# Kernel optimization log

Hardware: AMD Instinct MI355X
Metric: run time of the kernel (lower is better)

Reference implementation:

```python
import jax, jax.numpy as jnp
import numpy as np

DIM = 512; H = 8; HD = DIM // H
LAM = 4.0; NS_ITERS = 5; EPS = 1e-5
B = 2; S = 512


def setup_inputs() -> dict:
    key = jax.random.key(0)
    ks = jax.random.split(key, 3)
    return {
        "x": jax.random.normal(ks[0], (B, S, DIM), jnp.float32),
        "qkv_w": jax.random.normal(ks[1], (3 * DIM, DIM), jnp.float32) * 0.02,
        "qkv_b": jnp.zeros((3 * DIM,), jnp.float32),
        "proj_w": jax.random.normal(ks[2], (DIM, DIM), jnp.float32) * 0.02,
        "proj_b": jnp.zeros((DIM,), jnp.float32),
    }


def _ns_inverse(A, iters=NS_ITERS):
    # Newton-Schulz iterative matrix inverse: X <- X(2I - AX),
    # init X0 = A^T / (||A||_1 * ||A||_inf)
    n = A.shape[-1]
    I = jnp.eye(n, dtype=A.dtype)
    n1 = jnp.max(jnp.sum(jnp.abs(A), axis=-2), axis=-1)    # max column sum
    ninf = jnp.max(jnp.sum(jnp.abs(A), axis=-1), axis=-1)  # max row sum
    X = jnp.swapaxes(A, -2, -1) / (n1 * ninf)[..., None, None]
    for _ in range(iters):
        X = X @ (2.0 * I - A @ X)
    return X


def reference(x, qkv_w, qkv_b, proj_w, proj_b):
    Bb, Ss, C = x.shape
    qkv = x @ qkv_w.T + qkv_b                               # [B,S,3*DIM]
    qkv = qkv.reshape(Bb, Ss, 3, H, HD).transpose(2, 0, 3, 1, 4)
    q, k, v = qkv[0], qkv[1], qkv[2]                        # [B,H,S,HD]
    # Laplacian (L1) kernel: exp(-|q_i - k_j|_1 / lambda)
    l1 = jnp.sum(jnp.abs(q[:, :, :, None, :] - k[:, :, None, :, :]), axis=-1)
    W = jnp.exp(-l1 / LAM)                                  # [B,H,S,S]
    mask = jnp.tril(jnp.ones((Ss, Ss), dtype=x.dtype))      # causal mask
    W = W * mask
    W_inv = _ns_inverse(W)
    # whitening over (batch, query) dims; torch.var is unbiased (ddof=1)
    mu = jnp.mean(W, axis=(0, 2), keepdims=True)            # [1,H,1,S]
    var = jnp.var(W, axis=(0, 2), keepdims=True, ddof=1)
    W_norm = (W - mu) / jnp.sqrt(var + EPS)
    context = jnp.swapaxes(W, -2, -1) @ v                   # [B,H,S,HD]
    context = W_inv @ context
    ga = W_norm @ context                                   # [B,H,S,HD]
    ga = ga.transpose(0, 2, 1, 3).reshape(Bb, Ss, C)
    return ga @ proj_w.T + proj_b
```

## Files before the change

### kernel.cpp

```cpp
#include <hip/hip_runtime.h>

#define Bq 2
#define Hh 8
#define Ss 512
#define HD 64
#define DIM 512

using f32x4   = __attribute__((ext_vector_type(4))) float;
using bf16x8s = __attribute__((ext_vector_type(8))) short;
typedef _Float16 f16x8 __attribute__((ext_vector_type(8)));

__constant__ int d_tIs[36] = {0,1,1,2,2,2,3,3,3,3,4,4,4,4,4,5,5,5,5,5,5,6,6,6,6,6,6,6,7,7,7,7,7,7,7,7};
__constant__ int d_tJs[36] = {0,0,1,0,1,2,0,1,2,3,0,1,2,3,4,0,1,2,3,4,5,0,1,2,3,4,5,6,0,1,2,3,4,5,6,7};

__device__ __forceinline__ float bf2f(unsigned short u) {
    return __uint_as_float(((unsigned int)u) << 16);
}
__device__ __forceinline__ unsigned short f2bf(float f) {
    unsigned int u = __float_as_uint(f);
    u = (u + 0x7FFFu + ((u >> 16) & 1u)) >> 16;
    return (unsigned short)u;
}

__global__ __launch_bounds__(256) void mm64_k(
    const float* __restrict__ A, const float* __restrict__ B,
    const float* __restrict__ bias, float* __restrict__ C,
    int K, int ldc)
{
    const int row0 = blockIdx.y * 64, col0 = blockIdx.x * 64;
    __shared__ unsigned short AsH[64][40], AsL[64][40];
    __shared__ unsigned short BsH[64][40], BsL[64][40];
    const int t = threadIdx.x;
    const int wave = t >> 6, lane = t & 63;
    const int ln = lane & 15, quad = lane >> 4;

    f32x4 acc[4];
#pragma unroll
    for (int i = 0; i < 4; ++i) acc[i] = (f32x4){0.f, 0.f, 0.f, 0.f};

    const int sr = t >> 2, sg = (t & 3) * 8;

    for (int k0 = 0; k0 < K; k0 += 32) {
        __syncthreads();
#pragma unroll
        for (int half = 0; half < 2; ++half) {
            const float* src = half ? B : A;
            int base = half ? col0 : row0;
            const float* p = &src[(long)(base + sr) * K + k0 + sg];
            float4 f0 = *(const float4*)p;
            float4 f1 = *(const float4*)(p + 4);
            float fv[8] = {f0.x, f0.y, f0.z, f0.w, f1.x, f1.y, f1.z, f1.w};
            unsigned short hv[8], lv[8];
#pragma unroll
            for (int e = 0; e < 8; ++e) {
                hv[e] = f2bf(fv[e]);
                lv[e] = f2bf(fv[e] - bf2f(hv[e]));
            }
            uint4 H, L;
            H.x = hv[0] | (hv[1] << 16); H.y = hv[2] | (hv[3] << 16);
            H.z = hv[4] | (hv[5] << 16); H.w = hv[6] | (hv[7] << 16);
            L.x = lv[0] | (lv[1] << 16); L.y = lv[2] | (lv[3] << 16);
            L.z = lv[4] | (lv[5] << 16); L.w = lv[6] | (lv[7] << 16);
            if (!half) { *(uint4*)&AsH[sr][sg] = H; *(uint4*)&AsL[sr][sg] = L; }
            else       { *(uint4*)&BsH[sr][sg] = H; *(uint4*)&BsL[sr][sg] = L; }
        }
        __syncthreads();

        bf16x8s afH, afL, bfH[4], bfL[4];
        afH = *(const bf16x8s*)&AsH[wave * 16 + ln][quad * 8];
        afL = *(const bf16x8s*)&AsL[wave * 16 + ln][quad * 8];
#pragma unroll
        for (int nt = 0; nt < 4; ++nt) {
            bfH[nt] = *(const bf16x8s*)&BsH[nt * 16 + ln][quad * 8];
            bfL[nt] = *(const bf16x8s*)&BsL[nt * 16 + ln][quad * 8];
        }
#pragma unroll
        for (int nt = 0; nt < 4; ++nt) {
            acc[nt] = __builtin_amdgcn_mfma_f32_16x16x32_bf16(afH, bfH[nt], acc[nt], 0, 0, 0);
            acc[nt] = __builtin_amdgcn_mfma_f32_16x16x32_bf16(afH, bfL[nt], acc[nt], 0, 0, 0);
            acc[nt] = __builtin_amdgcn_mfma_f32_16x16x32_bf16(afL, bfH[nt], acc[nt], 0, 0, 0);
        }
    }

    const int gr0 = row0 + wave * 16 + quad * 4;
#pragma unroll
    for (int nt = 0; nt < 4; ++nt) {
        const int gc = col0 + nt * 16 + ln;
        float bb = bias[gc];
#pragma unroll
        for (int r = 0; r < 4; ++r)
            C[(long)(gr0 + r) * ldc + gc] = acc[nt][r] + bb;
    }
}

__global__ __launch_bounds__(256) void wt_fused(const float* __restrict__ qkv,
                                                _Float16* __restrict__ Wh,
                                                _Float16* __restrict__ Wt,
                                                _Float16* __restrict__ vT,
                                                float* __restrict__ rsum,
                                                float* __restrict__ rsq,
                                                float* __restrict__ csum)
{
    __shared__ float qs[32][64];
    __shared__ float ks[32][64];
    __shared__ float colacc[64];
    const int L = blockIdx.x;
    const int q = L & 7, s = L >> 3;
    const int z = 2 * q + (s >= 66 ? 1 : 0);
    const int bx = (s >= 66) ? s - 66 : s;
    int b = z >> 3, h = z & 7;
    int t = threadIdx.x;
    long zo = (long)z * Ss * Ss;

    if (bx >= 64) {
        float (*sT)[33] = (float(*)[33])qs;
        int dt = (bx - 64) * 32;
        int d = t & 31, kr = t >> 5;
        for (int kt = 0; kt < Ss; kt += 32) {
            __syncthreads();
#pragma unroll
            for (int p = 0; p < 4; ++p) {
                int kk = kr + p * 8;
                sT[kk][d] = qkv[(long)b * (Ss * 3 * DIM) + (long)(kt + kk) * (3 * DIM) + 2 * DIM + h * HD + dt + d];
            }
            __syncthreads();
#pragma unroll
            for (int p = 0; p < 4; ++p) {
                int dd = kr + p * 8;
                vT[(long)z * (HD * Ss) + (long)(dt + dd) * Ss + kt + d] = (_Float16)sT[d][dd];
            }
        }
        return;
    }

    int ti = bx >> 3, tj = bx & 7;
    int i0 = ti * 64, j0 = tj * 64;

    if (tj > ti) {
        if (t < 64) {
            rsum[((z * 8 + ti) * 512) + j0 + t] = 0.f;
            rsq [((z * 8 + ti) * 512) + j0 + t] = 0.f;
            csum[((z * 8 + tj) * 512) + i0 + t] = 0.f;
        }
        return;
    }

    int ia = (t & 15) * 4;
    int ja = (t >> 4) * 4;
    const float* qb = qkv + (long)b * Ss * (3 * DIM) + h * HD;
    const float* kb = qb + DIM;
    float acc[4][4] = {};

    for (int d0 = 0; d0 < 64; d0 += 32) {
        __syncthreads();
        int row = t & 63, dg = (t >> 6) * 8;
        float4 qv  = *(const float4*)&qb[(long)(i0 + row) * (3 * DIM) + d0 + dg];
        float4 qv2 = *(const float4*)&qb[(long)(i0 + row) * (3 * DIM) + d0 + dg + 4];
        float4 kv  = *(const float4*)&kb[(long)(j0 + row) * (3 * DIM) + d0 + dg];
        float4 kv2 = *(const float4*)&kb[(long)(j0 + row) * (3 * DIM) + d0 + dg + 4];
        qs[dg+0][row] = qv.x;  qs[dg+1][row] = qv.y;  qs[dg+2][row] = qv.z;  qs[dg+3][row] = qv.w;
        qs[dg+4][row] = qv2.x; qs[dg+5][row] = qv2.y; qs[dg+6][row] = qv2.z; qs[dg+7][row] = qv2.w;
        ks[dg+0][row] = kv.x;  ks[dg+1][row] = kv.y;  ks[dg+2][row] = kv.z;  ks[dg+3][row] = kv.w;
        ks[dg+4][row] = kv2.x; ks[dg+5][row] = kv2.y; ks[dg+6][row] = kv2.z; ks[dg+7][row] = kv2.w;
        __syncthreads();
#pragma unroll
        for (int d = 0; d < 32; ++d) {
            float4 q0 = *(const float4*)&qs[d][ia];
            float4 k0 = *(const float4*)&ks[d][ja];
            float qv_[4] = {q0.x, q0.y, q0.z, q0.w};
            float kv_[4] = {k0.x, k0.y, k0.z, k0.w};
#pragma unroll
            for (int aa = 0; aa < 4; ++aa)
#pragma unroll
                for (int c = 0; c < 4; ++c)
                    acc[aa][c] += fabsf(qv_[aa] - kv_[c]);
        }
    }

#pragma unroll
    for (int aa = 0; aa < 4; ++aa) {
        int i = i0 + ia + aa;
#pragma unroll
        for (int c = 0; c < 4; ++c) {
            int j = j0 + ja + c;
            float e = expf(-acc[aa][c] * 0.25f);
            acc[aa][c] = (j <= i) ? e : 0.0f;
        }
    }
#pragma unroll
    for (int c = 0; c < 4; ++c) {
        int j = j0 + ja + c;
        float rs = 0.f, rq = 0.f;
#pragma unroll
        for (int aa = 0; aa < 4; ++aa) { rs += acc[aa][c]; rq += acc[aa][c] * acc[aa][c]; }
        _Float16 ha[4] __attribute__((aligned(8))) = {(_Float16)acc[0][c], (_Float16)acc[1][c], (_Float16)acc[2][c], (_Float16)acc[3][c]};
        *(uint2*)&Wt[zo + (long)j * Ss + i0 + ia] = *(const uint2*)ha;
#pragma unroll
        for (int off = 8; off > 0; off >>= 1) {
            rs += __shfl_down(rs, off, 16);
            rq += __shfl_down(rq, off, 16);
        }
        if ((t & 15) == 0) {
            rsum[((z * 8 + ti) * 512) + j] = rs;
            rsq [((z * 8 + ti) * 512) + j] = rq;
        }
    }
#pragma unroll
    for (int aa = 0; aa < 4; ++aa) {
        int i = i0 + ia + aa;
        _Float16 hb[4] __attribute__((aligned(8))) = {(_Float16)acc[aa][0], (_Float16)acc[aa][1], (_Float16)acc[aa][2], (_Float16)acc[aa][3]};
        *(uint2*)&Wh[zo + (long)i * Ss + j0 + ja] = *(const uint2*)hb;
    }
    __syncthreads();
    if (t < 64) colacc[t] = 0.f;
    __syncthreads();
#pragma unroll
    for (int aa = 0; aa < 4; ++aa) {
        float cs = acc[aa][0] + acc[aa][1] + acc[aa][2] + acc[aa][3];
        atomicAdd(&colacc[ia + aa], cs);
    }
    __syncthreads();
    if (t < 64) csum[((z * 8 + tj) * 512) + i0 + t] = colacc[t];
}

__device__ __forceinline__ void wk_core(char* smc, const _Float16* A, const _Float16* B,
                                        long zA, long zB, int col0, int kbeg, int kend,
                                        f32x4* acc)
{
    _Float16 (*As0)[72] = (_Float16(*)[72])smc;
    _Float16 (*Bs0)[72] = (_Float16(*)[72])(smc + 9216);
    _Float16 (*As1)[72] = (_Float16(*)[72])(smc + 18432);
    _Float16 (*Bs1)[72] = (_Float16(*)[72])(smc + 27648);
    const int t = threadIdx.x;
    const int wave = t >> 6, lane = t & 63;
    const int ln = lane & 15, quad = lane >> 4;
    const int r2 = t >> 2, c2 = (t & 3) * 16;
    const long aoff = zA + (long)r2 * Ss;
    const long boff = zB + (long)(col0 + r2) * Ss;

    uint4 ua0 = *(const uint4*)&A[aoff + kbeg + c2];
    uint4 ua1 = *(const uint4*)&A[aoff + kbeg + c2 + 8];
    uint4 ub0 = *(const uint4*)&B[boff + kbeg + c2];
    uint4 ub1 = *(const uint4*)&B[boff + kbeg + c2 + 8];
    *(uint4*)&As0[r2][c2]     = ua0;
    *(uint4*)&As0[r2][c2 + 8] = ua1;
    *(uint4*)&Bs0[r2][c2]     = ub0;
    *(uint4*)&Bs0[r2][c2 + 8] = ub1;
    int cur = 0;
    for (int k0 = kbeg; k0 < kend; k0 += 64) {
        int kn = k0 + 64;
        if (kn < kend) {
            ua0 = *(const uint4*)&A[aoff + kn + c2];
            ua1 = *(const uint4*)&A[aoff + kn + c2 + 8];
            ub0 = *(const uint4*)&B[boff + kn + c2];
            ub1 = *(const uint4*)&B[boff + kn + c2 + 8];
        }
        __syncthreads();
        _Float16 (*As)[72] = cur ? As1 : As0;
        _Float16 (*Bs)[72] = cur ? Bs1 : Bs0;
#pragma unroll
        for (int kk = 0; kk < 64; kk += 32) {
            f16x8 af = *(const f16x8*)&As[wave * 16 + ln][quad * 8 + kk];
#pragma unroll
            for (int nt = 0; nt < 4; ++nt) {
                f16x8 bf = *(const f16x8*)&Bs[nt * 16 + ln][quad * 8 + kk];
                acc[nt] = __builtin_amdgcn_mfma_f32_16x16x32_f16(af, bf, acc[nt], 0, 0, 0);
            }
        }
        if (kn < kend) {
            _Float16 (*An)[72] = cur ? As0 : As1;
            _Float16 (*Bn)[72] = cur ? Bs0 : Bs1;
            *(uint4*)&An[r2][c2]     = ua0;
            *(uint4*)&An[r2][c2 + 8] = ua1;
            *(uint4*)&Bn[r2][c2]     = ub0;
            *(uint4*)&Bn[r2][c2 + 8] = ub1;
        }
        cur ^= 1;
    }
}

template<int HASA1>
__device__ __forceinline__ void wk_core32(char* smc, const float* A0, const float* A1,
                                          const _Float16* B, long zA, long zB, int col0,
                                          int kbeg, int kend, f32x4* acc)
{
    _Float16 (*As0)[40] = (_Float16(*)[40])smc;
    _Float16 (*Bs0)[40] = (_Float16(*)[40])(smc + 5120);
    _Float16 (*As1)[40] = (_Float16(*)[40])(smc + 10240);
    _Float16 (*Bs1)[40] = (_Float16(*)[40])(smc + 15360);
    const int t = threadIdx.x;
    const int wave = t >> 6, lane = t & 63;
    const int ln = lane & 15, quad = lane >> 4;
    const int r4 = t >> 2, c4 = (t & 3) * 8;
    const long aoff = zA + (long)r4 * Ss;
    const long boff = zB + (long)(col0 + r4) * Ss;

    float4 p0 = *(const float4*)&A0[aoff + kbeg + c4];
    float4 p1 = *(const float4*)&A0[aoff + kbeg + c4 + 4];
    float4 q0, q1;
    if constexpr (HASA1) {
        q0 = *(const float4*)&A1[aoff + kbeg + c4];
        q1 = *(const float4*)&A1[aoff + kbeg + c4 + 4];
    }
    uint4 ub = *(const uint4*)&B[boff + kbeg + c4];
    {
        _Float16 hv[8] __attribute__((aligned(16)));
        if constexpr (HASA1) {
            hv[0] = (_Float16)(p0.x + q0.x); hv[1] = (_Float16)(p0.y + q0.y);
            hv[2] = (_Float16)(p0.z + q0.z); hv[3] = (_Float16)(p0.w + q0.w);
            hv[4] = (_Float16)(p1.x + q1.x); hv[5] = (_Float16)(p1.y + q1.y);
            hv[6] = (_Float16)(p1.z + q1.z); hv[7] = (_Float16)(p1.w + q1.w);
        } else {
            hv[0] = (_Float16)p0.x; hv[1] = (_Float16)p0.y;
            hv[2] = (_Float16)p0.z; hv[3] = (_Float16)p0.w;
            hv[4] = (_Float16)p1.x; hv[5] = (_Float16)p1.y;
            hv[6] = (_Float16)p1.z; hv[7] = (_Float16)p1.w;
        }
        *(uint4*)&As0[r4][c4] = *(const uint4*)hv;
        *(uint4*)&Bs0[r4][c4] = ub;
    }
    int cur = 0;
    for (int k0 = kbeg; k0 < kend; k0 += 32) {
        int kn = k0 + 32;
        if (kn < kend) {
            p0 = *(const float4*)&A0[aoff + kn + c4];
            p1 = *(const float4*)&A0[aoff + kn + c4 + 4];
            if constexpr (HASA1) {
                q0 = *(const float4*)&A1[aoff + kn + c4];
                q1 = *(const float4*)&A1[aoff + kn + c4 + 4];
            }
            ub = *(const uint4*)&B[boff + kn + c4];
        }
        __syncthreads();
        _Float16 (*As)[40] = cur ? As1 : As0;
        _Float16 (*Bs)[40] = cur ? Bs1 : Bs0;
        f16x8 af = *(const f16x8*)&As[wave * 16 + ln][quad * 8];
#pragma unroll
        for (int nt = 0; nt < 4; ++nt) {
            f16x8 bf = *(const f16x8*)&Bs[nt * 16 + ln][quad * 8];
            acc[nt] = __builtin_amdgcn_mfma_f32_16x16x32_f16(af, bf, acc[nt], 0, 0, 0);
        }
        if (kn < kend) {
            _Float16 hv[8] __attribute__((aligned(16)));
            if constexpr (HASA1) {
                hv[0] = (_Float16)(p0.x + q0.x); hv[1] = (_Float16)(p0.y + q0.y);
                hv[2] = (_Float16)(p0.z + q0.z); hv[3] = (_Float16)(p0.w + q0.w);
                hv[4] = (_Float16)(p1.x + q1.x); hv[5] = (_Float16)(p1.y + q1.y);
                hv[6] = (_Float16)(p1.z + q1.z); hv[7] = (_Float16)(p1.w + q1.w);
            } else {
                hv[0] = (_Float16)p0.x; hv[1] = (_Float16)p0.y;
                hv[2] = (_Float16)p0.z; hv[3] = (_Float16)p0.w;
                hv[4] = (_Float16)p1.x; hv[5] = (_Float16)p1.y;
                hv[6] = (_Float16)p1.z; hv[7] = (_Float16)p1.w;
            }
            _Float16 (*An)[40] = cur ? As0 : As1;
            _Float16 (*Bn)[40] = cur ? Bs0 : Bs1;
            *(uint4*)&An[r4][c4] = *(const uint4*)hv;
            *(uint4*)&Bn[r4][c4] = ub;
        }
        cur ^= 1;
    }
}

__device__ __forceinline__ void sym_core(char* smc, const _Float16* A, long zo,
                                         int row0, int col0, int kend, f32x4* acc)
{
    _Float16 (*As0)[72] = (_Float16(*)[72])smc;
    _Float16 (*Bs0)[72] = (_Float16(*)[72])(smc + 9216);
    _Float16 (*As1)[72] = (_Float16(*)[72])(smc + 18432);
    _Float16 (*Bs1)[72] = (_Float16(*)[72])(smc + 27648);
    const int t = threadIdx.x;
    const int wave = t >> 6, lane = t & 63;
    const int ln = lane & 15, quad = lane >> 4;
    const int r2 = t >> 2, c2 = (t & 3) * 16;
    const long aoff = zo + (long)(row0 + r2) * Ss;
    const long boff = zo + (long)(col0 + r2) * Ss;
    uint4 ua0 = *(const uint4*)&A[aoff + c2];
    uint4 ua1 = *(const uint4*)&A[aoff + c2 + 8];
    uint4 ub0 = *(const uint4*)&A[boff + c2];
    uint4 ub1 = *(const uint4*)&A[boff + c2 + 8];
    *(uint4*)&As0[r2][c2]     = ua0;
    *(uint4*)&As0[r2][c2 + 8] = ua1;
    *(uint4*)&Bs0[r2][c2]     = ub0;
    *(uint4*)&Bs0[r2][c2 + 8] = ub1;
    int cur = 0;
    for (int k0 = 0; k0 < kend; k0 += 64) {
        int kn = k0 + 64;
        if (kn < kend) {
            ua0 = *(const uint4*)&A[aoff + kn + c2];
            ua1 = *(const uint4*)&A[aoff + kn + c2 + 8];
            ub0 = *(const uint4*)&A[boff + kn + c2];
            ub1 = *(const uint4*)&A[boff + kn + c2 + 8];
        }
        __syncthreads();
        _Float16 (*As)[72] = cur ? As1 : As0;
        _Float16 (*Bs)[72] = cur ? Bs1 : Bs0;
#pragma unroll
        for (int kk = 0; kk < 64; kk += 32) {
            f16x8 af = *(const f16x8*)&As[wave * 16 + ln][quad * 8 + kk];
#pragma unroll
            for (int nt = 0; nt < 4; ++nt) {
                f16x8 bf = *(const f16x8*)&Bs[nt * 16 + ln][quad * 8 + kk];
                acc[nt] = __builtin_amdgcn_mfma_f32_16x16x32_f16(af, bf, acc[nt], 0, 0, 0);
            }
        }
        if (kn < kend) {
            _Float16 (*An)[72] = cur ? As0 : As1;
            _Float16 (*Bn)[72] = cur ? Bs0 : Bs1;
            *(uint4*)&An[r2][c2]     = ua0;
            *(uint4*)&An[r2][c2 + 8] = ua1;
            *(uint4*)&Bn[r2][c2]     = ub0;
            *(uint4*)&Bn[r2][c2 + 8] = ub1;
        }
        cur ^= 1;
    }
}

__device__ __forceinline__ void sym_store_offdiag(char* smc, _Float16* T, long zo,
                                                  int row0, int col0,
                                                  const _Float16 (*ov)[4])
{
    _Float16 (*ltR)[72] = (_Float16(*)[72])smc;
    _Float16 (*ltT)[72] = (_Float16(*)[72])(smc + 9216);
    const int t = threadIdx.x;
    const int wave = t >> 6, lane = t & 63;
    const int ln = lane & 15, quad = lane >> 4;
    const int lr0 = wave * 16 + quad * 4;
    __syncthreads();
#pragma unroll
    for (int nt = 0; nt < 4; ++nt) {
        const int lc = nt * 16 + ln;
        *(uint2*)&ltT[lc][lr0] = *(const uint2*)ov[nt];
#pragma unroll
        for (int r = 0; r < 4; ++r)
            ltR[lr0 + r][lc] = ov[nt][r];
    }
    __syncthreads();
    const int tr = t >> 2, tcg = (t & 3) * 16;
    uint4 a0 = *(const uint4*)&ltR[tr][tcg];
    uint4 a1 = *(const uint4*)&ltR[tr][tcg + 8];
    _Float16* d0 = &T[zo + (long)(row0 + tr) * Ss + col0 + tcg];
    *(uint4*)&d0[0] = a0;
    *(uint4*)&d0[8] = a1;
    uint4 b0 = *(const uint4*)&ltT[tr][tcg];
    uint4 b1 = *(const uint4*)&ltT[tr][tcg + 8];
    _Float16* d1 = &T[zo + (long)(col0 + tr) * Ss + row0 + tcg];
    *(uint4*)&d1[0] = b0;
    *(uint4*)&d1[8] = b1;
}

__global__ __launch_bounds__(256) void mid_k(const _Float16* __restrict__ vT,
                                             const _Float16* __restrict__ Wt,
                                             float* __restrict__ y0,
                                             const float* __restrict__ rsum,
                                             const float* __restrict__ rsq,
                                             const float* __restrict__ csum,
                                             float* __restrict__ scal,
                                             float* __restrict__ mu,
                                             float* __restrict__ inv_sig,
                                             const _Float16* __restrict__ Wh,
                                             _Float16* __restrict__ U)
{
    __shared__ __align__(16) char sm[36864];
    int bx = blockIdx.x, t = threadIdx.x;
    if (bx < 128) {
        int q = bx & 7, s = bx >> 3;
        int z = 2 * q + (s >= 8 ? 1 : 0);
        int cc = s & 7;
        int col0 = cc * 64;
        long zA = (long)z * (HD * Ss), zB = (long)z * Ss * Ss;
        f32x4 acc[4];
#pragma unroll
        for (int i = 0; i < 4; ++i) acc[i] = (f32x4){0.f, 0.f, 0.f, 0.f};
        wk_core(sm, vT, Wt, zA, zB, col0, col0, Ss, acc);
        const int wave = t >> 6, lane = t & 63;
        const int ln = lane & 15, quad = lane >> 4;
        const int gr = wave * 16 + quad * 4;
#pragma unroll
        for (int nt = 0; nt < 4; ++nt) {
            const int gc = col0 + nt * 16 + ln;
#pragma unroll
            for (int r = 0; r < 4; ++r)
                y0[zA + (long)(gr + r) * Ss + gc] = acc[nt][r];
        }
    } else if (bx < 144) {
        int z = bx - 128;
        float* s1 = (float*)sm;
        float* s2 = s1 + 256;
        float mx1 = 0.f, mx2 = 0.f;
        for (int jj = t; jj < 512; jj += 256) {
            float rs = 0.f, cs = 0.f;
#pragma unroll
            for (int ti = 0; ti < 8; ++ti) {
                rs += rsum[(z * 8 + ti) * 512 + jj];
                cs += csum[(z * 8 + ti) * 512 + jj];
            }
            mx1 = fmaxf(mx1, rs);
            mx2 = fmaxf(mx2, cs);
        }
        s1[t] = mx1; s2[t] = mx2;
        __syncthreads();
        for (int off = 128; off > 0; off >>= 1) {
            if (t < off) {
                s1[t] = fmaxf(s1[t], s1[t + off]);
                s2[t] = fmaxf(s2[t], s2[t + off]);
            }
            __syncthreads();
        }
        if (t == 0) scal[z] = 1.0f / (s1[0] * s2[0]);
    } else if (bx < 152) {
        int h = bx - 144;
        for (int jj = t; jj < 512; jj += 256) {
            float s = 0.f, q = 0.f;
#pragma unroll
            for (int b = 0; b < 2; ++b)
#pragma unroll
                for (int ti = 0; ti < 8; ++ti) {
                    int zz = b * 8 + h;
                    s += rsum[(zz * 8 + ti) * 512 + jj];
                    q += rsq [(zz * 8 + ti) * 512 + jj];
                }
            float m_ = s / 1024.f;
            float var = (q - s * s / 1024.f) / 1023.f;
            inv_sig[h * 512 + jj] = 1.0f / sqrtf(var + 1e-5f);
            mu[h * 512 + jj] = m_;
        }
    } else {
        int u = bx - 152;
        int q = u & 7, s = u >> 3;
        int z = 2 * q + (s >= 36 ? 1 : 0);
        int tile = (s >= 36) ? s - 36 : s;
        const long zo = (long)z * Ss * Ss;
        const int ti = d_tIs[tile], tj = d_tJs[tile];
        const int row0 = ti * 64, col0 = tj * 64;
        f32x4 acc[4];
#pragma unroll
        for (int i = 0; i < 4; ++i) acc[i] = (f32x4){0.f, 0.f, 0.f, 0.f};
        sym_core(sm, Wh, zo, row0, col0, col0 + 64, acc);
        const int wave = t >> 6, lane = t & 63;
        const int ln = lane & 15, quad = lane >> 4;
        _Float16 ov[4][4] __attribute__((aligned(8)));
#pragma unroll
        for (int nt = 0; nt < 4; ++nt)
#pragma unroll
            for (int r = 0; r < 4; ++r)
                ov[nt][r] = (_Float16)acc[nt][r];
        if (ti == tj) {
            const int gr0 = row0 + wave * 16 + quad * 4;
#pragma unroll
            for (int nt = 0; nt < 4; ++nt) {
                const int gc = col0 + nt * 16 + ln;
#pragma unroll
                for (int r = 0; r < 4; ++r)
                    U[zo + (long)(gr0 + r) * Ss + gc] = ov[nt][r];
            }
        } else {
            sym_store_offdiag(sm, U, zo, row0, col0, ov);
        }
    }
}

template<int FIRST>
__global__ __launch_bounds__(256) void sq_k(const _Float16* __restrict__ Tc,
                                            _Float16* __restrict__ Tn,
                                            const float* __restrict__ Y0,
                                            const float* __restrict__ Y1,
                                            float* __restrict__ O0,
                                            float* __restrict__ O1,
                                            const float* __restrict__ scal)
{
    __shared__ __align__(16) char sm[36864];
    const int L = blockIdx.x;
    const int q = L & 7, s = L >> 3;
    const int z = 2 * q + (s >= 52 ? 1 : 0);
    const int x = (s >= 52) ? s - 52 : s;
    const int t = threadIdx.x;
    const int wave = t >> 6, lane = t & 63;
    const int ln = lane & 15, quad = lane >> 4;

    if (x < 36) {
        const long zo = (long)z * Ss * Ss;
        const int ti = d_tIs[x], tj = d_tJs[x];
        const int row0 = ti * 64, col0 = tj * 64;
        f32x4 acc[4];
#pragma unroll
        for (int i = 0; i < 4; ++i) acc[i] = (f32x4){0.f, 0.f, 0.f, 0.f};
        sym_core(sm, Tc, zo, row0, col0, Ss, acc);
        const float sv = FIRST ? scal[z] : 0.f;
        const int gr0 = row0 + wave * 16 + quad * 4;
        _Float16 ov[4][4] __attribute__((aligned(8)));
#pragma unroll
        for (int nt = 0; nt < 4; ++nt) {
            const int gc = col0 + nt * 16 + ln;
#pragma unroll
            for (int r = 0; r < 4; ++r) {
                const long gi = zo + (long)(gr0 + r) * Ss + gc;
                float val;
                if (FIRST) val = sv * sv * acc[nt][r] - 2.0f * sv * (float)Tc[gi];
                else       val = 2.0f * (float)Tc[gi] + acc[nt][r];
                ov[nt][r] = (_Float16)val;
            }
        }
        if (ti == tj) {
#pragma unroll
            for (int nt = 0; nt < 4; ++nt) {
                const int gc = col0 + nt * 16 + ln;
#pragma unroll
                for (int r = 0; r < 4; ++r)
                    Tn[zo + (long)(gr0 + r) * Ss + gc] = ov[nt][r];
            }
        } else {
            sym_store_offdiag(sm, Tn, zo, row0, col0, ov);
        }
    } else {
        const int bx = x - 36;
        const int cc = bx & 7, kh = bx >> 3;
        const int col0 = cc * 64;
        const long zA = (long)z * (HD * Ss);
        const long zB = (long)z * Ss * Ss;
        f32x4 acc[4];
#pragma unroll
        for (int i = 0; i < 4; ++i) acc[i] = (f32x4){0.f, 0.f, 0.f, 0.f};
        wk_core32<FIRST ? 0 : 1>(sm, Y0, Y1, Tc, zA, zB, col0, kh * 256, kh * 256 + 256, acc);
        const float alpha = FIRST ? -scal[z] : 1.0f;
        float* O = kh ? O1 : O0;
        const int gr = wave * 16 + quad * 4;
#pragma unroll
        for (int nt = 0; nt < 4; ++nt) {
            const int gc = col0 + nt * 16 + ln;
#pragma unroll
            for (int r = 0; r < 4; ++r) {
                const long idx = zA + (long)(gr + r) * Ss + gc;
                float val = alpha * acc[nt][r];
                if (kh == 0) {
                    if (FIRST) val += 2.0f * Y0[idx];
                    else       val += 2.0f * (Y0[idx] + Y1[idx]);
                }
                O[idx] = val;
            }
        }
    }
}

__global__ __launch_bounds__(256) void yk_k(const float* __restrict__ A0,
                                            const float* __restrict__ A1,
                                            const _Float16* __restrict__ T,
                                            float* __restrict__ O0,
                                            float* __restrict__ O1)
{
    __shared__ __align__(16) char sm[20480];
    const int L = blockIdx.x;
    const int q = L & 7, s = L >> 3;
    const int z = 2 * q + (s >= 16 ? 1 : 0);
    const int w = (s >= 16) ? s - 16 : s;
    const int cc = w & 7, kh = w >> 3;
    const int col0 = cc * 64;
    const long zA = (long)z * (HD * Ss);
    const long zB = (long)z * Ss * Ss;
    const int t = threadIdx.x;
    const int wave = t >> 6, lane = t & 63;
    const int ln = lane & 15, quad = lane >> 4;

    f32x4 acc[4];
#pragma unroll
    for (int i = 0; i < 4; ++i) acc[i] = (f32x4){0.f, 0.f, 0.f, 0.f};
    wk_core32<1>(sm, A0, A1, T, zA, zB, col0, kh * 256, kh * 256 + 256, acc);

    float* O = kh ? O1 : O0;
    const int gr = wave * 16 + quad * 4;
#pragma unroll
    for (int nt = 0; nt < 4; ++nt) {
        const int gc = col0 + nt * 16 + ln;
#pragma unroll
        for (int r = 0; r < 4; ++r) {
            const long idx = zA + (long)(gr + r) * Ss + gc;
            float val = acc[nt][r];
            if (kh == 0) val += 2.0f * (A0[idx] + A1[idx]);
            O[idx] = val;
        }
    }
}

__global__ __launch_bounds__(256) void c2s_k(const float* __restrict__ A0,
                                             const float* __restrict__ A1,
                                             const _Float16* __restrict__ Wt,
                                             _Float16* __restrict__ c2sT,
                                             const float* __restrict__ scal,
                                             const float* __restrict__ inv_sig,
                                             const float* __restrict__ mu,
                                             float* __restrict__ negopart)
{
    __shared__ __align__(16) char sm[20480];
    __shared__ float red[64];
    const int L = blockIdx.x;
    const int q = L & 7, sIdx = L >> 3;
    const int z = 2 * q + (sIdx >= 8 ? 1 : 0);
    const int cb = (sIdx >= 8) ? sIdx - 8 : sIdx;
    const int h = z & 7;
    const int col0 = cb * 64;
    const long zA = (long)z * (HD * Ss);
    const long zB = (long)z * Ss * Ss;
    const int t = threadIdx.x;
    const int wave = t >> 6, lane = t & 63;
    const int ln = lane & 15, quad = lane >> 4;

    f32x4 acc[4];
#pragma unroll
    for (int i = 0; i < 4; ++i) acc[i] = (f32x4){0.f, 0.f, 0.f, 0.f};
    wk_core32<1>(sm, A0, A1, Wt, zA, zB, col0, col0, Ss, acc);

    if (t < 64) red[t] = 0.f;
    __syncthreads();
    const int gr = wave * 16 + quad * 4;
    float pr[4] = {0.f, 0.f, 0.f, 0.f};
    float s = scal[z];
#pragma unroll
    for (int nt = 0; nt < 4; ++nt) {
        const int gc = col0 + nt * 16 + ln;
#pragma unroll
        for (int r = 0; r < 4; ++r) {
            float val = inv_sig[h * 512 + gc] * (s * acc[nt][r]);
            pr[r] += mu[h * 512 + gc] * val;
            c2sT[zA + (long)(gr + r) * Ss + gc] = (_Float16)val;
        }
    }
#pragma unroll
    for (int r = 0; r < 4; ++r)
        atomicAdd(&red[gr + r], pr[r]);
    __syncthreads();
    if (t < 64)
        negopart[(z * 8 + cb) * 64 + t] = red[t];
}

__global__ __launch_bounds__(256) void ga_k(const _Float16* __restrict__ Wh,
                                            const _Float16* __restrict__ c2sT,
                                            const float* __restrict__ negopart,
                                            float* __restrict__ gat)
{
    __shared__ __align__(16) char sm[36864];
    __shared__ float neg[64];
    const int L = blockIdx.x;
    const int q = L & 7, sIdx = L >> 3;
    const int z = 2 * q + (sIdx >= 8 ? 1 : 0);
    const int mb = (sIdx >= 8) ? sIdx - 8 : sIdx;
    const int b = z >> 3, h = z & 7;
    const int m0 = mb * 64;
    const long zA = (long)z * Ss * Ss;
    const long zB = (long)z * (HD * Ss);
    const int t = threadIdx.x;
    const int wave = t >> 6, lane = t & 63;
    const int ln = lane & 15, quad = lane >> 4;

    if (t < 64) {
        float s = 0.f;
#pragma unroll
        for (int k = 0; k < 8; ++k) s += negopart[(z * 8 + k) * 64 + t];
        neg[t] = s;
    }
    __syncthreads();

    f32x4 acc[4];
#pragma unroll
    for (int i = 0; i < 4; ++i) acc[i] = (f32x4){0.f, 0.f, 0.f, 0.f};
    wk_core(sm, c2sT, Wh, zB, zA, m0, 0, m0 + 64, acc);

    const int gr = wave * 16 + quad * 4;
#pragma unroll
    for (int nt = 0; nt < 4; ++nt) {
        const int m = m0 + nt * 16 + ln;
#pragma unroll
        for (int r = 0; r < 4; ++r) {
            const int d = gr + r;
            gat[(long)b * (Ss * DIM) + (long)m * DIM + h * HD + d] = acc[nt][r] - neg[d];
        }
    }
}

extern "C" void kernel_launch(void* const* d_in, const int* in_sizes, int n_in,
                              void* d_out, int out_size, void* d_ws, size_t ws_size,
                              hipStream_t stream)
{
    const float* x      = (const float*)d_in[0];
    const float* qkv_w  = (const float*)d_in[1];
    const float* qkv_b  = (const float*)d_in[2];
    const float* proj_w = (const float*)d_in[3];
    const float* proj_b = (const float*)d_in[4];
    float* out = (float*)d_out;
    float* ws  = (float*)d_ws;

    float* qkv     = ws;
    _Float16* Wh   = (_Float16*)(ws + 1572864);
    _Float16* Wt   = (_Float16*)(ws + 3670016);
    _Float16* vT   = (_Float16*)(ws + 5767168);
    _Float16* T[5];
    for (int i = 0; i < 5; ++i) T[i] = (_Float16*)(ws + 6029312 + (long)i * 2097152);
    float* Ya0 = ws + 16515072;
    float* Ya1 = ws + 17039360;
    float* Yb0 = ws + 17563648;
    float* Yb1 = ws + 18087936;
    _Float16* c2sT = (_Float16*)(ws + 19136512);
    float* rsum    = ws + 19398656;
    float* rsq     = ws + 19464192;
    float* csum    = ws + 19529728;
    float* scal    = ws + 19595264;
    float* mu      = ws + 19595280;
    float* inv_sig = ws + 19599376;
    float* negp    = ws + 19603472;
    float* gat     = ws + 19611664;

    dim3 blk(256);

    mm64_k<<<dim3(24, 16), blk, 0, stream>>>(x, qkv_w, qkv_b, qkv, DIM, 3 * DIM);

    wt_fused<<<dim3(1056), blk, 0, stream>>>(qkv, Wh, Wt, vT, rsum, rsq, csum);

    mid_k<<<dim3(728), blk, 0, stream>>>(vT, Wt, Ya0, rsum, rsq, csum, scal, mu, inv_sig,
                                         Wh, T[0]);

    sq_k<1><<<dim3(832), blk, 0, stream>>>(T[0], T[1], Ya0, nullptr, Yb0, Yb1, scal);
    sq_k<0><<<dim3(832), blk, 0, stream>>>(T[1], T[2], Yb0, Yb1,     Ya0, Ya1, scal);
    sq_k<0><<<dim3(832), blk, 0, stream>>>(T[2], T[3], Ya0, Ya1,     Yb0, Yb1, scal);
    sq_k<0><<<dim3(832), blk, 0, stream>>>(T[3], T[4], Yb0, Yb1,     Ya0, Ya1, scal);

    yk_k<<<dim3(256), blk, 0, stream>>>(Ya0, Ya1, T[4], Yb0, Yb1);

    c2s_k<<<dim3(128), blk, 0, stream>>>(Yb0, Yb1, Wt, c2sT, scal, inv_sig, mu, negp);

    ga_k<<<dim3(128), blk, 0, stream>>>(Wh, c2sT, negp, gat);

    mm64_k<<<dim3(8, 16), blk, 0, stream>>>(gat, proj_w, proj_b, out, DIM, DIM);
}
```

Baseline: 198.6 us.

## Launch only lower-triangular W tiles and widen wk_core32 K-step to 64

The W-building kernel now launches only the 36 causal (lower-triangular plus diagonal) 64x64 tiles per head, using lookup tables, instead of 64 tiles with early exit. Upper tiles no longer exist as blocks, so each lower-triangle block also zeroes the transposed partial-sum slots. The shared wk_core32 GEMM loop now stages 64-wide K chunks with a 72-element padded shared layout, halving the number of barrier and load phases. The price is more shared memory per block (36 KB) and more registers for prefetch buffers, which may reduce occupancy.

```diff
diff --git a/kernel.cpp b/kernel.cpp
--- a/kernel.cpp
+++ b/kernel.cpp
@@ -106,15 +106,15 @@
     __shared__ float colacc[64];
     const int L = blockIdx.x;
     const int q = L & 7, s = L >> 3;
-    const int z = 2 * q + (s >= 66 ? 1 : 0);
-    const int bx = (s >= 66) ? s - 66 : s;
+    const int z = 2 * q + (s >= 38 ? 1 : 0);
+    const int bx = (s >= 38) ? s - 38 : s;
     int b = z >> 3, h = z & 7;
     int t = threadIdx.x;
     long zo = (long)z * Ss * Ss;
 
-    if (bx >= 64) {
+    if (bx >= 36) {
         float (*sT)[33] = (float(*)[33])qs;
-        int dt = (bx - 64) * 32;
+        int dt = (bx - 36) * 32;
         int d = t & 31, kr = t >> 5;
         for (int kt = 0; kt < Ss; kt += 32) {
             __syncthreads();
@@ -133,16 +133,13 @@
         return;
     }
 
-    int ti = bx >> 3, tj = bx & 7;
-    int i0 = ti * 64, j0 = tj * 64;
-
-    if (tj > ti) {
-        if (t < 64) {
-            rsum[((z * 8 + ti) * 512) + j0 + t] = 0.f;
-            rsq [((z * 8 + ti) * 512) + j0 + t] = 0.f;
-            csum[((z * 8 + tj) * 512) + i0 + t] = 0.f;
-        }
-        return;
+    const int ti = d_tIs[bx], tj = d_tJs[bx];
+    const int i0 = ti * 64, j0 = tj * 64;
+
+    if (ti > tj && t < 64) {
+        rsum[((z * 8 + tj) * 512) + i0 + t] = 0.f;
+        rsq [((z * 8 + tj) * 512) + i0 + t] = 0.f;
+        csum[((z * 8 + ti) * 512) + j0 + t] = 0.f;
     }
 
     int ia = (t & 15) * 4;
@@ -284,79 +281,77 @@
                                           const _Float16* B, long zA, long zB, int col0,
                                           int kbeg, int kend, f32x4* acc)
 {
-    _Float16 (*As0)[40] = (_Float16(*)[40])smc;
-    _Float16 (*Bs0)[40] = (_Float16(*)[40])(smc + 5120);
-    _Float16 (*As1)[40] = (_Float16(*)[40])(smc + 10240);
-    _Float16 (*Bs1)[40] = (_Float16(*)[40])(smc + 15360);
+    _Float16 (*As0)[72] = (_Float16(*)[72])smc;
+    _Float16 (*Bs0)[72] = (_Float16(*)[72])(smc + 9216);
+    _Float16 (*As1)[72] = (_Float16(*)[72])(smc + 18432);
+    _Float16 (*Bs1)[72] = (_Float16(*)[72])(smc + 27648);
     const int t = threadIdx.x;
     const int wave = t >> 6, lane = t & 63;
     const int ln = lane & 15, quad = lane >> 4;
-    const int r4 = t >> 2, c4 = (t & 3) * 8;
-    const long aoff = zA + (long)r4 * Ss;
-    const long boff = zB + (long)(col0 + r4) * Ss;
-
-    float4 p0 = *(const float4*)&A0[aoff + kbeg + c4];
-    float4 p1 = *(const float4*)&A0[aoff + kbeg + c4 + 4];
-    float4 q0, q1;
+    const int r2 = t >> 2, c2 = (t & 3) * 16;
+    const long aoff = zA + (long)r2 * Ss;
+    const long boff = zB + (long)(col0 + r2) * Ss;
+
+    float pa[16], qa[16];
+    uint4 ub0, ub1;
+#pragma unroll
+    for (int e = 0; e < 4; ++e)
+        *(float4*)&pa[e * 4] = *(const float4*)&A0[aoff + kbeg + c2 + e * 4];
     if constexpr (HASA1) {
-        q0 = *(const float4*)&A1[aoff + kbeg + c4];
-        q1 = *(const float4*)&A1[aoff + kbeg + c4 + 4];
-    }
-    uint4 ub = *(const uint4*)&B[boff + kbeg + c4];
+#pragma unroll
+        for (int e = 0; e < 4; ++e)
+            *(float4*)&qa[e * 4] = *(const float4*)&A1[aoff + kbeg + c2 + e * 4];
+    }
+    ub0 = *(const uint4*)&B[boff + kbeg + c2];
+    ub1 = *(const uint4*)&B[boff + kbeg + c2 + 8];
     {
-        _Float16 hv[8] __attribute__((aligned(16)));
-        if constexpr (HASA1) {
-            hv[0] = (_Float16)(p0.x + q0.x); hv[1] = (_Float16)(p0.y + q0.y);
-            hv[2] = (_Float16)(p0.z + q0.z); hv[3] = (_Float16)(p0.w + q0.w);
-            hv[4] = (_Float16)(p1.x + q1.x); hv[5] = (_Float16)(p1.y + q1.y);
-            hv[6] = (_Float16)(p1.z + q1.z); hv[7] = (_Float16)(p1.w + q1.w);
-        } else {
-            hv[0] = (_Float16)p0.x; hv[1] = (_Float16)p0.y;
-            hv[2] = (_Float16)p0.z; hv[3] = (_Float16)p0.w;
-            hv[4] = (_Float16)p1.x; hv[5] = (_Float16)p1.y;
-            hv[6] = (_Float16)p1.z; hv[7] = (_Float16)p1.w;
-        }
-        *(uint4*)&As0[r4][c4] = *(const uint4*)hv;
-        *(uint4*)&Bs0[r4][c4] = ub;
+        _Float16 hv[16] __attribute__((aligned(16)));
+#pragma unroll
+        for (int e = 0; e < 16; ++e)
+            hv[e] = HASA1 ? (_Float16)(pa[e] + qa[e]) : (_Float16)pa[e];
+        *(uint4*)&As0[r2][c2]     = *(const uint4*)&hv[0];
+        *(uint4*)&As0[r2][c2 + 8] = *(const uint4*)&hv[8];
+        *(uint4*)&Bs0[r2][c2]     = ub0;
+        *(uint4*)&Bs0[r2][c2 + 8] = ub1;
     }
     int cur = 0;
-    for (int k0 = kbeg; k0 < kend; k0 += 32) {
-        int kn = k0 + 32;
+    for (int k0 = kbeg; k0 < kend; k0 += 64) {
+        int kn = k0 + 64;
         if (kn < kend) {
-            p0 = *(const float4*)&A0[aoff + kn + c4];
-            p1 = *(const float4*)&A0[aoff + kn + c4 + 4];
+#pragma unroll
+            for (int e = 0; e < 4; ++e)
+                *(float4*)&pa[e * 4] = *(const float4*)&A0[aoff + kn + c2 + e * 4];
             if constexpr (HASA1) {
-                q0 = *(const float4*)&A1[aoff + kn + c4];
-                q1 = *(const float4*)&A1[aoff + kn + c4 + 4];
-            }
-            ub = *(const uint4*)&B[boff + kn + c4];
+#pragma unroll
+                for (int e = 0; e < 4; ++e)
+                    *(float4*)&qa[e * 4] = *(const float4*)&A1[aoff + kn + c2 + e * 4];
+            }
+            ub0 = *(const uint4*)&B[boff + kn + c2];
+            ub1 = *(const uint4*)&B[boff + kn + c2 + 8];
         }
         __syncthreads();
-        _Float16 (*As)[40] = cur ? As1 : As0;
-        _Float16 (*Bs)[40] = cur ? Bs1 : Bs0;
-        f16x8 af = *(const f16x8*)&As[wave * 16 + ln][quad * 8];
-#pragma unroll
-        for (int nt = 0; nt < 4; ++nt) {
-            f16x8 bf = *(const f16x8*)&Bs[nt * 16 + ln][quad * 8];
-            acc[nt] = __builtin_amdgcn_mfma_f32_16x16x32_f16(af, bf, acc[nt], 0, 0, 0);
+        _Float16 (*As)[72] = cur ? As1 : As0;
+        _Float16 (*Bs)[72] = cur ? Bs1 : Bs0;
+#pragma unroll
+        for (int kk = 0; kk < 64; kk += 32) {
+            f16x8 af = *(const f16x8*)&As[wave * 16 + ln][quad * 8 + kk];
+#pragma unroll
+            for (int nt = 0; nt < 4; ++nt) {
+                f16x8 bf = *(const f16x8*)&Bs[nt * 16 + ln][quad * 8 + kk];
+                acc[nt] = __builtin_amdgcn_mfma_f32_16x16x32_f16(af, bf, acc[nt], 0, 0, 0);
+            }
         }
         if (kn < kend) {
-            _Float16 hv[8] __attribute__((aligned(16)));
-            if constexpr (HASA1) {
-                hv[0] = (_Float16)(p0.x + q0.x); hv[1] = (_Float16)(p0.y + q0.y);
-                hv[2] = (_Float16)(p0.z + q0.z); hv[3] = (_Float16)(p0.w + q0.w);
-                hv[4] = (_Float16)(p1.x + q1.x); hv[5] = (_Float16)(p1.y + q1.y);
-                hv[6] = (_Float16)(p1.z + q1.z); hv[7] = (_Float16)(p1.w + q1.w);
-            } else {
-                hv[0] = (_Float16)p0.x; hv[1] = (_Float16)p0.y;
-                hv[2] = (_Float16)p0.z; hv[3] = (_Float16)p0.w;
-                hv[4] = (_Float16)p1.x; hv[5] = (_Float16)p1.y;
-                hv[6] = (_Float16)p1.z; hv[7] = (_Float16)p1.w;
-            }
-            _Float16 (*An)[40] = cur ? As0 : As1;
-            _Float16 (*Bn)[40] = cur ? Bs0 : Bs1;
-            *(uint4*)&An[r4][c4] = *(const uint4*)hv;
-            *(uint4*)&Bn[r4][c4] = ub;
+            _Float16 hv[16] __attribute__((aligned(16)));
+#pragma unroll
+            for (int e = 0; e < 16; ++e)
+                hv[e] = HASA1 ? (_Float16)(pa[e] + qa[e]) : (_Float16)pa[e];
+            _Float16 (*An)[72] = cur ? As0 : As1;
+            _Float16 (*Bn)[72] = cur ? Bs0 : Bs1;
+            *(uint4*)&An[r2][c2]     = *(const uint4*)&hv[0];
+            *(uint4*)&An[r2][c2 + 8] = *(const uint4*)&hv[8];
+            *(uint4*)&Bn[r2][c2]     = ub0;
+            *(uint4*)&Bn[r2][c2 + 8] = ub1;
         }
         cur ^= 1;
     }
@@ -648,7 +643,7 @@
                                             float* __restrict__ O0,
                                             float* __restrict__ O1)
 {
-    __shared__ __align__(16) char sm[20480];
+    __shared__ __align__(16) char sm[36864];
     const int L = blockIdx.x;
     const int q = L & 7, s = L >> 3;
     const int z = 2 * q + (s >= 16 ? 1 : 0);
@@ -690,7 +685,7 @@
                                              const float* __restrict__ mu,
                                              float* __restrict__ negopart)
 {
-    __shared__ __align__(16) char sm[20480];
+    __shared__ __align__(16) char sm[36864];
     __shared__ float red[64];
     const int L = blockIdx.x;
     const int q = L & 7, sIdx = L >> 3;
@@ -812,7 +807,7 @@
 
     mm64_k<<<dim3(24, 16), blk, 0, stream>>>(x, qkv_w, qkv_b, qkv, DIM, 3 * DIM);
 
-    wt_fused<<<dim3(1056), blk, 0, stream>>>(qkv, Wh, Wt, vT, rsum, rsq, csum);
+    wt_fused<<<dim3(608), blk, 0, stream>>>(qkv, Wh, Wt, vT, rsum, rsq, csum);
 
     mid_k<<<dim3(728), blk, 0, stream>>>(vT, Wt, Ya0, rsum, rsq, csum, scal, mu, inv_sig,
                                          Wh, T[0]);
```

Result: no change. 195.6 us (-1.5%).
